# Performance work log

Hardware: AMD Instinct MI355X
Metric: run time of the kernel (lower is better)

The kernel has to match this reference:

```python
import jax, jax.numpy as jnp
import numpy as np

N, E = 50000, 800000
IN_DIM, HID, H1, H2, NCLS = 512, 64, 4, 1, 40
NEG_SLOPE = 0.2


def gat_conv(x, src, dst, W, att_src, att_dst, b, heads, ch):
    # x: [N, F_in]; W: [F_in, heads*ch]; att_*: [heads, ch]; b: [heads*ch]
    n = x.shape[0]
    h = (x @ W).reshape(n, heads, ch)                      # [N,H,C]
    a_s = jnp.einsum('nhc,hc->nh', h, att_src)             # [N,H]
    a_d = jnp.einsum('nhc,hc->nh', h, att_dst)             # [N,H]
    e = jax.nn.leaky_relu(a_s[src] + a_d[dst], NEG_SLOPE)  # [E,H]
    # segment softmax over incoming edges of each destination node
    m = jax.ops.segment_max(e, dst, num_segments=n)        # [N,H]
    ex = jnp.exp(e - m[dst])
    s = jax.ops.segment_sum(ex, dst, num_segments=n)       # [N,H]
    alpha = ex / (s[dst] + 1e-16)                          # [E,H]
    out = jax.ops.segment_sum(alpha[:, :, None] * h[src], dst, num_segments=n)
    return out.reshape(n, heads * ch) + b


def setup_inputs() -> dict:
    key = jax.random.key(0)
    ks = jax.random.split(key, 10)
    glorot = lambda k, shp: jax.random.normal(k, shp, jnp.float32) * jnp.sqrt(2.0 / (shp[0] + shp[-1]))
    return {
        'x': jax.random.normal(ks[0], (N, IN_DIM), jnp.float32),
        'edge_index': jax.random.randint(ks[1], (2, E), 0, N, jnp.int64),
        'W1': glorot(ks[2], (IN_DIM, H1 * HID)),
        'att_src1': glorot(ks[3], (H1, HID)),
        'att_dst1': glorot(ks[4], (H1, HID)),
        'b1': jnp.zeros((H1 * HID,), jnp.float32),
        'W2': glorot(ks[5], (H1 * HID, H2 * NCLS)),
        'att_src2': glorot(ks[6], (H2, NCLS)),
        'att_dst2': glorot(ks[7], (H2, NCLS)),
        'b2': jnp.zeros((H2 * NCLS,), jnp.float32),
    }


def reference(x, edge_index, W1, att_src1, att_dst1, b1, W2, att_src2, att_dst2, b2):
    n = x.shape[0]
    loops = jnp.arange(n, dtype=edge_index.dtype)
    src = jnp.concatenate([edge_index[0], loops])  # add self loops (PyG default)
    dst = jnp.concatenate([edge_index[1], loops])
    # dropout layers are identity in eval mode
    h = gat_conv(x, src, dst, W1, att_src1, att_dst1, b1, H1, HID)
    h = jax.nn.elu(h)
    out = gat_conv(h, src, dst, W2, att_src2, att_dst2, b2, H2, NCLS)
    return jax.nn.log_softmax(out, axis=1)
```

## Files before the change

### kernel.cpp

```cpp
#include <hip/hip_runtime.h>
#include <math.h>
#include <stdint.h>


typedef short bf16x8 __attribute__((ext_vector_type(8)));
typedef float f32x4  __attribute__((ext_vector_type(4)));

static __device__ __forceinline__ float leaky(float x){ return x > 0.f ? x : 0.2f*x; }
static __device__ __forceinline__ unsigned short f2bf(float f){
  uint32_t u = __float_as_uint(f);
  uint32_t r = u + 0x7fffu + ((u >> 16) & 1u);
  return (unsigned short)(r >> 16);
}
static __device__ __forceinline__ float bf2f(unsigned short u){
  return __uint_as_float(((uint32_t)u) << 16);
}

__global__ void k_cvt_w(const float* __restrict__ W, unsigned short* __restrict__ wt,
                        int* __restrict__ deg, int n){
  int i = blockIdx.x*blockDim.x + threadIdx.x;
  if (i < n) deg[i] = 0;
  if (i >= 512*256) return;
  int k = i >> 8, c = i & 255;
  wt[c*512 + k] = f2bf(W[i]);
}

__global__ void k_count(const int* __restrict__ ei, int E, int n, int* __restrict__ deg){
  int i = blockIdx.x*blockDim.x + threadIdx.x;
  int tot = E + n;
  if (i >= tot) return;
  int dst = (i < E) ? ei[E + i] : (i - E);
  atomicAdd(&deg[dst], 1);
}

__global__ __launch_bounds__(256) void k_scan_a(const int* __restrict__ deg,
    int* __restrict__ rowstart, int* __restrict__ bsum, int n){
  __shared__ int sm[256];
  int b = blockIdx.x, t = threadIdx.x;
  int i = b*256 + t;
  int v = (i < n) ? deg[i] : 0;
  sm[t] = v;
  __syncthreads();
  for (int off=1; off<256; off<<=1){
    int u = (t >= off) ? sm[t-off] : 0;
    __syncthreads();
    sm[t] += u;
    __syncthreads();
  }
  if (i < n) rowstart[i+1] = sm[t];
  if (t == 255) bsum[b] = sm[255];
}
__global__ __launch_bounds__(256) void k_scan_b(int* __restrict__ bsum, int nb){
  __shared__ int sm[256];
  int t = threadIdx.x;
  int v = (t < nb) ? bsum[t] : 0;
  sm[t] = v;
  __syncthreads();
  for (int off=1; off<256; off<<=1){
    int u = (t >= off) ? sm[t-off] : 0;
    __syncthreads();
    sm[t] += u;
    __syncthreads();
  }
  if (t < nb) bsum[t] = sm[t] - v;
}
__global__ __launch_bounds__(256) void k_scan_c(int* __restrict__ rowstart,
    const int* __restrict__ bsum, int* __restrict__ cur, int n){
  int b = blockIdx.x, t = threadIdx.x;
  int i = b*256 + t;
  if (i < n){ rowstart[i+1] += bsum[b]; cur[i] = 0; }
  if (i == 0) rowstart[0] = 0;
}

__global__ __launch_bounds__(256) void k_gemm1_mfma(const float* __restrict__ X,
                                                    const unsigned short* __restrict__ BT,
                                                    const float* __restrict__ SW,
                                                    const float* __restrict__ DW,
                                                    unsigned short* __restrict__ Cb,
                                                    float* __restrict__ as1,
                                                    float* __restrict__ ad1, int M){
  __shared__ __align__(16) unsigned short lA[4*128*8];
  __shared__ __align__(16) unsigned short lB[4*128*8];
  const int t = threadIdx.x;
  const int lane = t & 63, w = t >> 6;
  const int wx = w & 1, wy = w >> 1;
  const int row0 = blockIdx.x * 128, col0 = blockIdx.y * 128;

  f32x4 acc[4][4];
  #pragma unroll
  for (int i=0;i<4;i++)
    #pragma unroll
    for (int j=0;j<4;j++)
      #pragma unroll
      for (int r=0;r<4;r++) acc[i][j][r] = 0.f;

  const int c0 = t, c1 = t + 256;
  const int r0 = c0 & 127, kq0 = c0 >> 7;
  const int r1 = c1 & 127, kq1 = c1 >> 7;
  const float* xA0 = X + (size_t)min(row0 + r0, M-1)*512 + kq0*8;
  const float* xA1 = X + (size_t)min(row0 + r1, M-1)*512 + kq1*8;
  const size_t gB0 = (size_t)(col0 + r0)*512 + kq0*8;
  const size_t gB1 = (size_t)(col0 + r1)*512 + kq1*8;

  const int kq = lane >> 4, li = lane & 15;

  for (int kt = 0; kt < 512; kt += 32){
    __builtin_amdgcn_global_load_lds((const __attribute__((address_space(1))) void*)(BT + gB0 + kt),
        (__attribute__((address_space(3))) void*)&lB[c0*8], 16, 0, 0);
    __builtin_amdgcn_global_load_lds((const __attribute__((address_space(1))) void*)(BT + gB1 + kt),
        (__attribute__((address_space(3))) void*)&lB[c1*8], 16, 0, 0);
    float4 a00 = *(const float4*)(xA0 + kt);
    float4 a01 = *(const float4*)(xA0 + kt + 4);
    float4 a10 = *(const float4*)(xA1 + kt);
    float4 a11 = *(const float4*)(xA1 + kt + 4);
    bf16x8 p0, p1;
    p0[0]=(short)f2bf(a00.x); p0[1]=(short)f2bf(a00.y); p0[2]=(short)f2bf(a00.z); p0[3]=(short)f2bf(a00.w);
    p0[4]=(short)f2bf(a01.x); p0[5]=(short)f2bf(a01.y); p0[6]=(short)f2bf(a01.z); p0[7]=(short)f2bf(a01.w);
    p1[0]=(short)f2bf(a10.x); p1[1]=(short)f2bf(a10.y); p1[2]=(short)f2bf(a10.z); p1[3]=(short)f2bf(a10.w);
    p1[4]=(short)f2bf(a11.x); p1[5]=(short)f2bf(a11.y); p1[6]=(short)f2bf(a11.z); p1[7]=(short)f2bf(a11.w);
    *(bf16x8*)&lA[c0*8] = p0;
    *(bf16x8*)&lA[c1*8] = p1;
    __syncthreads();

    bf16x8 af[4], bfr[4];
    #pragma unroll
    for (int i=0;i<4;i++){
      af[i]  = *(const bf16x8*)&lA[(kq*128 + wx*64 + i*16 + li)*8];
      bfr[i] = *(const bf16x8*)&lB[(kq*128 + wy*64 + i*16 + li)*8];
    }
    #pragma unroll
    for (int i=0;i<4;i++)
      #pragma unroll
      for (int j=0;j<4;j++)
        acc[i][j] = __builtin_amdgcn_mfma_f32_16x16x32_bf16(af[i], bfr[j], acc[i][j], 0, 0, 0);
    __syncthreads();
  }

  #pragma unroll
  for (int i=0;i<4;i++){
    #pragma unroll
    for (int r=0;r<4;r++){
      int row = row0 + wx*64 + i*16 + kq*4 + r;
      if (row < M){
        #pragma unroll
        for (int j=0;j<4;j++)
          Cb[(size_t)row*256 + col0 + wy*64 + j*16 + li] = f2bf(acc[i][j][r]);
      }
    }
  }

  const int hw = (int)blockIdx.y*2 + wy;
  float sv[4], dv[4];
  #pragma unroll
  for (int j=0;j<4;j++){
    sv[j] = SW[hw*64 + j*16 + li];
    dv[j] = DW[hw*64 + j*16 + li];
  }
  #pragma unroll
  for (int i=0;i<4;i++){
    #pragma unroll
    for (int r=0;r<4;r++){
      float ps = acc[i][0][r]*sv[0] + acc[i][1][r]*sv[1] + acc[i][2][r]*sv[2] + acc[i][3][r]*sv[3];
      float pd = acc[i][0][r]*dv[0] + acc[i][1][r]*dv[1] + acc[i][2][r]*dv[2] + acc[i][3][r]*dv[3];
      #pragma unroll
      for (int o=1;o<16;o<<=1){ ps += __shfl_xor(ps,o); pd += __shfl_xor(pd,o); }
      int row = row0 + wx*64 + i*16 + kq*4 + r;
      if (li == 0 && row < M){
        as1[row*4 + hw] = ps;
        ad1[row*4 + hw] = pd;
      }
    }
  }
}

__global__ void k_fill(const int* __restrict__ ei, int E, int n,
                       const int* __restrict__ rowstart, int* __restrict__ cur,
                       int* __restrict__ csr,
                       const float* __restrict__ as1, const float* __restrict__ ad1,
                       float* __restrict__ exbuf){
  int i = blockIdx.x*blockDim.x + threadIdx.x;
  int tot = E + n;
  if (i >= tot) return;
  int src, dst;
  if (i < E){ src = ei[i]; dst = ei[E+i]; } else { src = i - E; dst = src; }
  int pos = atomicAdd(&cur[dst], 1);
  int slot = rowstart[dst] + pos;
  csr[slot] = src;
  float4 a = *(const float4*)(as1 + (size_t)src*4);
  float4 d = *(const float4*)(ad1 + (size_t)dst*4);
  float4 ex;
  ex.x = __expf(fminf(leaky(a.x + d.x), 80.f));
  ex.y = __expf(fminf(leaky(a.y + d.y), 80.f));
  ex.z = __expf(fminf(leaky(a.z + d.z), 80.f));
  ex.w = __expf(fminf(leaky(a.w + d.w), 80.f));
  *(float4*)(exbuf + (size_t)slot*4) = ex;
}

__global__ __launch_bounds__(256) void k_agg1(const unsigned short* __restrict__ h1b,
    const float* __restrict__ exbuf,
    const int* __restrict__ rowstart, const int* __restrict__ csr,
    const float* __restrict__ b1, unsigned short* __restrict__ hactb, int n){
  int lane = threadIdx.x & 63;
  int node = blockIdx.x*4 + (threadIdx.x >> 6);
  if (node >= n) return;
  int lo = __builtin_amdgcn_readfirstlane(rowstart[node]);
  int hi = __builtin_amdgcn_readfirstlane(rowstart[node+1]);
  int h = lane >> 4;
  const float* exb = exbuf + h;
  float ax=0.f, ay=0.f, az=0.f, aw=0.f, psum=0.f;
  int e = lo;
  for (; e + 7 < hi; e += 8){
    int s0 = csr[e],   s1 = csr[e+1], s2 = csr[e+2], s3 = csr[e+3];
    int s4 = csr[e+4], s5 = csr[e+5], s6 = csr[e+6], s7 = csr[e+7];
    float e0 = exb[(size_t)e*4],     e1 = exb[(size_t)(e+1)*4],
          e2 = exb[(size_t)(e+2)*4], e3 = exb[(size_t)(e+3)*4],
          e4 = exb[(size_t)(e+4)*4], e5 = exb[(size_t)(e+5)*4],
          e6 = exb[(size_t)(e+6)*4], e7 = exb[(size_t)(e+7)*4];
    ushort4 u0 = *(const ushort4*)(h1b + (size_t)s0*256 + lane*4);
    ushort4 u1 = *(const ushort4*)(h1b + (size_t)s1*256 + lane*4);
    ushort4 u2 = *(const ushort4*)(h1b + (size_t)s2*256 + lane*4);
    ushort4 u3 = *(const ushort4*)(h1b + (size_t)s3*256 + lane*4);
    ushort4 u4 = *(const ushort4*)(h1b + (size_t)s4*256 + lane*4);
    ushort4 u5 = *(const ushort4*)(h1b + (size_t)s5*256 + lane*4);
    ushort4 u6 = *(const ushort4*)(h1b + (size_t)s6*256 + lane*4);
    ushort4 u7 = *(const ushort4*)(h1b + (size_t)s7*256 + lane*4);
    ax += e0*bf2f(u0.x) + e1*bf2f(u1.x) + e2*bf2f(u2.x) + e3*bf2f(u3.x)
        + e4*bf2f(u4.x) + e5*bf2f(u5.x) + e6*bf2f(u6.x) + e7*bf2f(u7.x);
    ay += e0*bf2f(u0.y) + e1*bf2f(u1.y) + e2*bf2f(u2.y) + e3*bf2f(u3.y)
        + e4*bf2f(u4.y) + e5*bf2f(u5.y) + e6*bf2f(u6.y) + e7*bf2f(u7.y);
    az += e0*bf2f(u0.z) + e1*bf2f(u1.z) + e2*bf2f(u2.z) + e3*bf2f(u3.z)
        + e4*bf2f(u4.z) + e5*bf2f(u5.z) + e6*bf2f(u6.z) + e7*bf2f(u7.z);
    aw += e0*bf2f(u0.w) + e1*bf2f(u1.w) + e2*bf2f(u2.w) + e3*bf2f(u3.w)
        + e4*bf2f(u4.w) + e5*bf2f(u5.w) + e6*bf2f(u6.w) + e7*bf2f(u7.w);
    psum += (e0+e1+e2+e3) + (e4+e5+e6+e7);
  }
  for (; e < hi; ++e){
    int s0 = csr[e];
    float e0 = exb[(size_t)e*4];
    ushort4 u0 = *(const ushort4*)(h1b + (size_t)s0*256 + lane*4);
    ax += e0*bf2f(u0.x); ay += e0*bf2f(u0.y); az += e0*bf2f(u0.z); aw += e0*bf2f(u0.w);
    psum += e0;
  }
  float inv = 1.f/(psum + 1e-16f);
  float4 bv = *(const float4*)(b1 + lane*4);
  float o0 = ax*inv + bv.x, o1 = ay*inv + bv.y, o2 = az*inv + bv.z, o3 = aw*inv + bv.w;
  ushort4 r;
  r.x = f2bf(o0 > 0.f ? o0 : expm1f(o0));
  r.y = f2bf(o1 > 0.f ? o1 : expm1f(o1));
  r.z = f2bf(o2 > 0.f ? o2 : expm1f(o2));
  r.w = f2bf(o3 > 0.f ? o3 : expm1f(o3));
  *(ushort4*)(hactb + (size_t)node*256 + lane*4) = r;
}

__global__ __launch_bounds__(256) void k_gemm2(const unsigned short* __restrict__ A,
    const float* __restrict__ B, const float* __restrict__ sw, const float* __restrict__ dw,
    unsigned short* __restrict__ Cb, float* __restrict__ as2, float* __restrict__ ad2, int M){
  __shared__ float Xl[32][129];
  __shared__ float Wl[128*40];
  __shared__ float Sps[32][8], Spd[32][8];
  int t = threadIdx.x;
  int row0 = blockIdx.x*32;
  int r = t & 31, g = t >> 5;
  float acc[5] = {0,0,0,0,0};
  for (int kt=0; kt<256; kt+=128){
    for (int i=t; i<1280; i+=256)
      *(float4*)&Wl[i*4] = *(const float4*)(B + kt*40 + i*4);
    for (int i=t; i<512; i+=256){
      int rr = i >> 4, k8 = i & 15;
      int grow = row0 + rr; if (grow >= M) grow = M-1;
      uint4 v = *(const uint4*)(A + (size_t)grow*256 + kt + k8*8);
      float* xp = &Xl[rr][k8*8];
      xp[0] = __uint_as_float(v.x << 16); xp[1] = __uint_as_float(v.x & 0xffff0000u);
      xp[2] = __uint_as_float(v.y << 16); xp[3] = __uint_as_float(v.y & 0xffff0000u);
      xp[4] = __uint_as_float(v.z << 16); xp[5] = __uint_as_float(v.z & 0xffff0000u);
      xp[6] = __uint_as_float(v.w << 16); xp[7] = __uint_as_float(v.w & 0xffff0000u);
    }
    __syncthreads();
    #pragma unroll 4
    for (int k=0;k<128;++k){
      float a = Xl[r][k];
      const float* wp = &Wl[k*40 + g*5];
      #pragma unroll
      for (int j=0;j<5;++j) acc[j] += a * wp[j];
    }
    __syncthreads();
  }
  int grow = row0 + r;
  float ps = 0.f, pd = 0.f;
  #pragma unroll
  for (int j=0;j<5;++j){
    ps += acc[j] * sw[g*5+j];
    pd += acc[j] * dw[g*5+j];
  }
  Sps[r][g] = ps; Spd[r][g] = pd;
  if (grow < M){
    #pragma unroll
    for (int j=0;j<5;++j) Cb[(size_t)grow*40 + g*5 + j] = f2bf(acc[j]);
  }
  __syncthreads();
  if (t < 32){
    float a = 0.f, b = 0.f;
    #pragma unroll
    for (int g2=0; g2<8; ++g2){ a += Sps[t][g2]; b += Spd[t][g2]; }
    int rw = row0 + t;
    if (rw < M){ as2[rw] = a; ad2[rw] = b; }
  }
}

__global__ __launch_bounds__(256) void k_pre2(const float* __restrict__ as2,
    const float* __restrict__ ad2, const int* __restrict__ rowstart,
    const int* __restrict__ csr, float* __restrict__ ex2, int n){
  int lane = threadIdx.x & 63;
  int node = blockIdx.x*4 + (threadIdx.x >> 6);
  if (node >= n) return;
  int lo = rowstart[node], hi = rowstart[node+1];
  float adn = ad2[node];
  for (int e = lo + lane; e < hi; e += 64)
    ex2[e] = __expf(fminf(leaky(as2[csr[e]] + adn), 80.f));
}

__global__ __launch_bounds__(256) void k_agg2(const unsigned short* __restrict__ h2b,
    const float* __restrict__ ex2,
    const int* __restrict__ rowstart, const int* __restrict__ csr,
    const float* __restrict__ b2, float* __restrict__ out, int n){
  int lane = threadIdx.x & 63;
  int node = blockIdx.x*4 + (threadIdx.x >> 6);
  if (node >= n) return;
  int lo = __builtin_amdgcn_readfirstlane(rowstart[node]);
  int hi = __builtin_amdgcn_readfirstlane(rowstart[node+1]);
  bool act = lane < 40;
  float acc = 0.f, psum = 0.f;
  int e = lo;
  for (; e + 7 < hi; e += 8){
    int s0 = csr[e],   s1 = csr[e+1], s2 = csr[e+2], s3 = csr[e+3];
    int s4 = csr[e+4], s5 = csr[e+5], s6 = csr[e+6], s7 = csr[e+7];
    float e0 = ex2[e],   e1 = ex2[e+1], e2 = ex2[e+2], e3 = ex2[e+3];
    float e4 = ex2[e+4], e5 = ex2[e+5], e6 = ex2[e+6], e7 = ex2[e+7];
    float h0 = act ? bf2f(h2b[(size_t)s0*40 + lane]) : 0.f;
    float h1 = act ? bf2f(h2b[(size_t)s1*40 + lane]) : 0.f;
    float h2 = act ? bf2f(h2b[(size_t)s2*40 + lane]) : 0.f;
    float h3 = act ? bf2f(h2b[(size_t)s3*40 + lane]) : 0.f;
    float h4 = act ? bf2f(h2b[(size_t)s4*40 + lane]) : 0.f;
    float h5 = act ? bf2f(h2b[(size_t)s5*40 + lane]) : 0.f;
    float h6 = act ? bf2f(h2b[(size_t)s6*40 + lane]) : 0.f;
    float h7 = act ? bf2f(h2b[(size_t)s7*40 + lane]) : 0.f;
    acc += e0*h0 + e1*h1 + e2*h2 + e3*h3 + e4*h4 + e5*h5 + e6*h6 + e7*h7;
    psum += (e0+e1+e2+e3) + (e4+e5+e6+e7);
  }
  for (; e < hi; ++e){
    int s0 = csr[e]; float e0 = ex2[e];
    acc += e0 * (act ? bf2f(h2b[(size_t)s0*40 + lane]) : 0.f);
    psum += e0;
  }
  float ov = acc/(psum + 1e-16f) + (act ? b2[lane] : 0.f);
  float v = act ? ov : -INFINITY;
  float mx = v;
  #pragma unroll
  for (int o=1;o<64;o<<=1) mx = fmaxf(mx, __shfl_xor(mx,o));
  float ev = act ? __expf(ov - mx) : 0.f;
  float se = ev;
  #pragma unroll
  for (int o=1;o<64;o<<=1) se += __shfl_xor(se,o);
  if (act) out[(size_t)node*40 + lane] = (ov - mx) - __logf(se);
}

extern "C" void kernel_launch(void* const* d_in, const int* in_sizes, int n_in,
                              void* d_out, int out_size, void* d_ws, size_t ws_size,
                              hipStream_t stream){
  const float* x   = (const float*)d_in[0];
  const int*   ei  = (const int*)d_in[1];
  const float* W1  = (const float*)d_in[2];
  const float* s1w = (const float*)d_in[3];
  const float* d1w = (const float*)d_in[4];
  const float* b1  = (const float*)d_in[5];
  const float* W2  = (const float*)d_in[6];
  const float* s2w = (const float*)d_in[7];
  const float* d2w = (const float*)d_in[8];
  const float* b2  = (const float*)d_in[9];
  float* out = (float*)d_out;

  const int N  = in_sizes[0] / 512;
  const int E  = in_sizes[1] / 2;
  const int Et = E + N;

  float* f = (float*)d_ws;
  unsigned short* h1b   = (unsigned short*)f;  f += (size_t)N*128;
  unsigned short* hactb = (unsigned short*)f;  f += (size_t)N*128;
  float* as1  = f;  f += (size_t)N*4;
  float* ad1  = f;  f += (size_t)N*4;
  float* as2  = f;  f += N;
  float* ad2  = f;  f += N;
  unsigned short* w1t = (unsigned short*)f;  f += 256*512/2;
  unsigned short* h2b = (unsigned short*)f;  f += (size_t)N*40/2 + 64;
  float* exbuf = f;  f += (size_t)Et*4;
  float* ex2   = f;  f += Et;
  int* ip = (int*)f;
  int* rowstart = ip;  ip += (N + 4) & ~3;
  int* deg      = ip;  ip += N;
  int* cur      = ip;  ip += N;
  int* csr      = ip;  ip += Et;
  int* bsum     = ip;  ip += 256;

  int nb4 = (N + 3) / 4;
  int nbs = (N + 255) / 256;
  k_cvt_w<<<512, 256, 0, stream>>>(W1, w1t, deg, N);
  k_count<<<(Et+255)/256, 256, 0, stream>>>(ei, E, N, deg);
  k_scan_a<<<nbs, 256, 0, stream>>>(deg, rowstart, bsum, N);
  k_scan_b<<<1, 256, 0, stream>>>(bsum, nbs);
  k_scan_c<<<nbs, 256, 0, stream>>>(rowstart, bsum, cur, N);
  k_gemm1_mfma<<<dim3((N+127)/128, 2), 256, 0, stream>>>(x, w1t, s1w, d1w, h1b, as1, ad1, N);
  k_fill <<<(Et+255)/256, 256, 0, stream>>>(ei, E, N, rowstart, cur, csr, as1, ad1, exbuf);
  k_agg1 <<<nb4, 256, 0, stream>>>(h1b, exbuf, rowstart, csr, b1, hactb, N);
  k_gemm2<<<(N+31)/32, 256, 0, stream>>>(hactb, W2, s2w, d2w, h2b, as2, ad2, N);
  k_pre2 <<<nb4, 256, 0, stream>>>(as2, ad2, rowstart, csr, ex2, N);
  k_agg2 <<<nb4, 256, 0, stream>>>(h2b, ex2, rowstart, csr, b2, out, N);
}
```

Measured before the change: 471.6 us.

## Double-buffer LDS tiles in layer-1 GEMM to overlap loads with MFMA

Converts the layer-1 bf16 MFMA GEMM's K loop into a double-buffered pipeline. The next tile's X loads and async B global-to-LDS loads are issued before the current tile's MFMAs, and the conversion and write into the alternate buffer happens after them. This leaves one barrier per K step instead of two. It also adds a launch-bounds occupancy hint of 3 blocks per CU, which doubles LDS use and may raise register pressure or spill.

Measured after the change: 470.1 us. Within noise of the previous version (-0.3%).

```diff
diff --git a/kernel.cpp b/kernel.cpp
--- a/kernel.cpp
+++ b/kernel.cpp
@@ -72,15 +72,15 @@
   if (i == 0) rowstart[0] = 0;
 }
 
-__global__ __launch_bounds__(256) void k_gemm1_mfma(const float* __restrict__ X,
+__global__ __launch_bounds__(256, 3) void k_gemm1_mfma(const float* __restrict__ X,
                                                     const unsigned short* __restrict__ BT,
                                                     const float* __restrict__ SW,
                                                     const float* __restrict__ DW,
                                                     unsigned short* __restrict__ Cb,
                                                     float* __restrict__ as1,
                                                     float* __restrict__ ad1, int M){
-  __shared__ __align__(16) unsigned short lA[4*128*8];
-  __shared__ __align__(16) unsigned short lB[4*128*8];
+  __shared__ __align__(16) unsigned short lA[2][4096];
+  __shared__ __align__(16) unsigned short lB[2][4096];
   const int t = threadIdx.x;
   const int lane = t & 63, w = t >> 6;
   const int wx = w & 1, wy = w >> 1;
@@ -99,42 +99,72 @@
   const int r1 = c1 & 127, kq1 = c1 >> 7;
   const float* xA0 = X + (size_t)min(row0 + r0, M-1)*512 + kq0*8;
   const float* xA1 = X + (size_t)min(row0 + r1, M-1)*512 + kq1*8;
-  const size_t gB0 = (size_t)(col0 + r0)*512 + kq0*8;
-  const size_t gB1 = (size_t)(col0 + r1)*512 + kq1*8;
+  const unsigned short* bB0 = BT + (size_t)(col0 + r0)*512 + kq0*8;
+  const unsigned short* bB1 = BT + (size_t)(col0 + r1)*512 + kq1*8;
 
   const int kq = lane >> 4, li = lane & 15;
 
-  for (int kt = 0; kt < 512; kt += 32){
-    __builtin_amdgcn_global_load_lds((const __attribute__((address_space(1))) void*)(BT + gB0 + kt),
-        (__attribute__((address_space(3))) void*)&lB[c0*8], 16, 0, 0);
-    __builtin_amdgcn_global_load_lds((const __attribute__((address_space(1))) void*)(BT + gB1 + kt),
-        (__attribute__((address_space(3))) void*)&lB[c1*8], 16, 0, 0);
-    float4 a00 = *(const float4*)(xA0 + kt);
-    float4 a01 = *(const float4*)(xA0 + kt + 4);
-    float4 a10 = *(const float4*)(xA1 + kt);
-    float4 a11 = *(const float4*)(xA1 + kt + 4);
-    bf16x8 p0, p1;
-    p0[0]=(short)f2bf(a00.x); p0[1]=(short)f2bf(a00.y); p0[2]=(short)f2bf(a00.z); p0[3]=(short)f2bf(a00.w);
-    p0[4]=(short)f2bf(a01.x); p0[5]=(short)f2bf(a01.y); p0[6]=(short)f2bf(a01.z); p0[7]=(short)f2bf(a01.w);
-    p1[0]=(short)f2bf(a10.x); p1[1]=(short)f2bf(a10.y); p1[2]=(short)f2bf(a10.z); p1[3]=(short)f2bf(a10.w);
-    p1[4]=(short)f2bf(a11.x); p1[5]=(short)f2bf(a11.y); p1[6]=(short)f2bf(a11.z); p1[7]=(short)f2bf(a11.w);
-    *(bf16x8*)&lA[c0*8] = p0;
-    *(bf16x8*)&lA[c1*8] = p1;
-    __syncthreads();
-
-    bf16x8 af[4], bfr[4];
-    #pragma unroll
-    for (int i=0;i<4;i++){
-      af[i]  = *(const bf16x8*)&lA[(kq*128 + wx*64 + i*16 + li)*8];
-      bfr[i] = *(const bf16x8*)&lB[(kq*128 + wy*64 + i*16 + li)*8];
-    }
-    #pragma unroll
-    for (int i=0;i<4;i++)
-      #pragma unroll
-      for (int j=0;j<4;j++)
-        acc[i][j] = __builtin_amdgcn_mfma_f32_16x16x32_bf16(af[i], bfr[j], acc[i][j], 0, 0, 0);
-    __syncthreads();
-  }
+#define ISSUE_B(NXT, KTB) do{ \
+  __builtin_amdgcn_global_load_lds((const __attribute__((address_space(1))) void*)(bB0 + (KTB)), \
+      (__attribute__((address_space(3))) void*)&lB[NXT][c0*8], 16, 0, 0); \
+  __builtin_amdgcn_global_load_lds((const __attribute__((address_space(1))) void*)(bB1 + (KTB)), \
+      (__attribute__((address_space(3))) void*)&lB[NXT][c1*8], 16, 0, 0); }while(0)
+
+#define CVT_WRITE(NXT, S0,S1,S2,S3) do{ \
+  bf16x8 p0, p1; \
+  p0[0]=(short)f2bf(S0.x); p0[1]=(short)f2bf(S0.y); p0[2]=(short)f2bf(S0.z); p0[3]=(short)f2bf(S0.w); \
+  p0[4]=(short)f2bf(S1.x); p0[5]=(short)f2bf(S1.y); p0[6]=(short)f2bf(S1.z); p0[7]=(short)f2bf(S1.w); \
+  p1[0]=(short)f2bf(S2.x); p1[1]=(short)f2bf(S2.y); p1[2]=(short)f2bf(S2.z); p1[3]=(short)f2bf(S2.w); \
+  p1[4]=(short)f2bf(S3.x); p1[5]=(short)f2bf(S3.y); p1[6]=(short)f2bf(S3.z); p1[7]=(short)f2bf(S3.w); \
+  *(bf16x8*)&lA[NXT][c0*8] = p0; \
+  *(bf16x8*)&lA[NXT][c1*8] = p1; }while(0)
+
+#define STEP(T, CUR) do{ \
+  float4 n0, n1, n2, n3; \
+  if ((T) < 15){ \
+    const int ktn = ((T)+1)*32; \
+    n0 = *(const float4*)(xA0 + ktn); \
+    n1 = *(const float4*)(xA0 + ktn + 4); \
+    n2 = *(const float4*)(xA1 + ktn); \
+    n3 = *(const float4*)(xA1 + ktn + 4); \
+    ISSUE_B((CUR)^1, ktn); \
+  } \
+  bf16x8 af[4], bfr[4]; \
+  _Pragma("unroll") \
+  for (int i=0;i<4;i++){ \
+    af[i]  = *(const bf16x8*)&lA[CUR][(kq*128 + wx*64 + i*16 + li)*8]; \
+    bfr[i] = *(const bf16x8*)&lB[CUR][(kq*128 + wy*64 + i*16 + li)*8]; \
+  } \
+  _Pragma("unroll") \
+  for (int i=0;i<4;i++) \
+    _Pragma("unroll") \
+    for (int j=0;j<4;j++) \
+      acc[i][j] = __builtin_amdgcn_mfma_f32_16x16x32_bf16(af[i], bfr[j], acc[i][j], 0, 0, 0); \
+  if ((T) < 15){ \
+    CVT_WRITE((CUR)^1, n0, n1, n2, n3); \
+    __syncthreads(); \
+  } \
+}while(0)
+
+  {
+    float4 a0 = *(const float4*)(xA0);
+    float4 a1 = *(const float4*)(xA0 + 4);
+    float4 a2 = *(const float4*)(xA1);
+    float4 a3 = *(const float4*)(xA1 + 4);
+    ISSUE_B(0, 0);
+    CVT_WRITE(0, a0, a1, a2, a3);
+    __syncthreads();
+  }
+
+  #pragma unroll
+  for (int tt = 0; tt < 8; ++tt){
+    STEP(2*tt,   (0));
+    STEP(2*tt+1, (1));
+  }
+
+#undef STEP
+#undef CVT_WRITE
+#undef ISSUE_B
 
   #pragma unroll
   for (int i=0;i<4;i++){
```
